# Optimization experiments

Measured on AMD Instinct MI355X. Metric: run time of the kernel, lower is better.

Reference implementation:

```python
import jax, jax.numpy as jnp
import numpy as np
import math

B, T, D = 4, 8192, 1024
EPS = 1e-5

def setup_inputs() -> dict:
    key = jax.random.key(0)
    ks = jax.random.split(key, 8)
    xavier = lambda k, shape: jax.random.uniform(k, shape, jnp.float32,
                                                 -math.sqrt(6.0 / (shape[0] + shape[1])),
                                                 math.sqrt(6.0 / (shape[0] + shape[1])))
    x = jax.random.normal(ks[0], (B, T, D), jnp.float32)
    ln_gamma = jnp.ones((D,), jnp.float32)
    ln_beta = jnp.zeros((D,), jnp.float32)
    Wg = xavier(ks[1], (D, D))            # torch Linear weight: (out, in)
    bg = jnp.zeros((D,), jnp.float32)
    Wv = 0.01 * xavier(ks[2], (D, D))     # gain=0.01
    bv = jnp.zeros((D,), jnp.float32)
    Wo = 0.01 * xavier(ks[3], (D, D))     # gain=0.01
    bo = jnp.zeros((D,), jnp.float32)
    log_decay = jnp.asarray(math.log(math.exp(0.01) - 1.0), jnp.float32)
    return {"x": x, "ln_gamma": ln_gamma, "ln_beta": ln_beta,
            "Wg": Wg, "bg": bg, "Wv": Wv, "bv": bv, "Wo": Wo, "bo": bo,
            "log_decay": log_decay}

def reference(x, ln_gamma, ln_beta, Wg, bg, Wv, bv, Wo, bo, log_decay):
    # LayerNorm
    mu = jnp.mean(x, axis=-1, keepdims=True)
    var = jnp.mean(jnp.square(x - mu), axis=-1, keepdims=True)
    normed = (x - mu) * jax.lax.rsqrt(var + EPS) * ln_gamma + ln_beta
    # gate / value projections (torch Linear: y = x @ W.T + b)
    g = jax.nn.sigmoid(jnp.einsum('btd,ed->bte', normed, Wg) + bg)
    v = jnp.einsum('btd,ed->bte', normed, Wv) + bv
    # push-pull cumulative sums over time
    cumsum = jnp.cumsum(g * v, axis=1) - jnp.cumsum((1.0 - g) * v, axis=1)
    # positional exponential decay
    alpha = jax.nn.softplus(log_decay)
    positions = jnp.arange(x.shape[1], dtype=jnp.float32)
    decay = jnp.exp(-alpha * positions)[None, :, None]  # (1,T,1)
    out = jnp.einsum('btd,ed->bte', cumsum * decay, Wo) + bo
    return x + out  # dropout is identity at eval
```

## Files before the change

kernel.cpp:

```cpp
#include <hip/hip_runtime.h>
#include <cstdint>
#include <cstddef>

#define DD 1024
#define TT 8192
#define BB 4
#define MM (BB*TT)
#define NCHUNK 64
#define CLEN 128
#define EPS 1e-5f
#define NKT 32

typedef __attribute__((ext_vector_type(8))) short bf16x8;
typedef __attribute__((ext_vector_type(4))) float f32x4;

__device__ __forceinline__ float bf2f(unsigned short b) {
  union { unsigned int u; float f; } c; c.u = ((unsigned int)b) << 16; return c.f;
}
__device__ __forceinline__ unsigned short f2bf(float f) {
  union { float f; unsigned int u; } c; c.f = f;
  unsigned int lsb = (c.u >> 16) & 1u;
  c.u += 0x7fffu + lsb;
  return (unsigned short)(c.u >> 16);
}

__device__ __forceinline__ void gload16(const void* gsrc, void* ldst) {
  __builtin_amdgcn_global_load_lds(
      (const __attribute__((address_space(1))) unsigned int*)gsrc,
      (__attribute__((address_space(3))) unsigned int*)ldst, 16, 0, 0);
}

#define SWZ(row) (((row) >> 1) & 3)

__device__ __forceinline__ bf16x8 ldsfrag(const unsigned short* lds, int row, int sl) {
  int sp = sl ^ SWZ(row);
  return *(const bf16x8*)&lds[row * 32 + sp * 8];
}

#define MFMA16(a, b, c) __builtin_amdgcn_mfma_f32_16x16x32_bf16((a), (b), (c), 0, 0, 0)

#define VMCNT0 asm volatile("s_waitcnt vmcnt(0)" ::: "memory")
#define BAR    __builtin_amdgcn_s_barrier()

__global__ __launch_bounds__(256) void cast_weights(
    const float* __restrict__ wg, const float* __restrict__ wv,
    const float* __restrict__ wo,
    unsigned short* __restrict__ owg, unsigned short* __restrict__ owv,
    unsigned short* __restrict__ owo) {
  int i = blockIdx.x * 256 + threadIdx.x;
  const float* src; unsigned short* dst; int off;
  if (i < 262144)       { src = wg; dst = owg; off = i; }
  else if (i < 524288)  { src = wv; dst = owv; off = i - 262144; }
  else                  { src = wo; dst = owo; off = i - 524288; }
  float4 v = ((const float4*)src)[off];
  ushort4 o;
  o.x = f2bf(v.x); o.y = f2bf(v.y); o.z = f2bf(v.z); o.w = f2bf(v.w);
  ((ushort4*)dst)[off] = o;
}

__global__ __launch_bounds__(256) void ln_kernel(
    const float* __restrict__ x, const float* __restrict__ gamma,
    const float* __restrict__ beta, unsigned short* __restrict__ normed) {
  size_t row = blockIdx.x;
  int tid = threadIdx.x, lane = tid & 63, wid = tid >> 6;
  float4 v = ((const float4*)(x + row * DD))[tid];
  float s = v.x + v.y + v.z + v.w;
  float q = v.x * v.x + v.y * v.y + v.z * v.z + v.w * v.w;
#pragma unroll
  for (int off = 32; off; off >>= 1) {
    s += __shfl_down(s, off);
    q += __shfl_down(q, off);
  }
  __shared__ float rs[4], rq[4];
  if (lane == 0) { rs[wid] = s; rq[wid] = q; }
  __syncthreads();
  float ts = rs[0] + rs[1] + rs[2] + rs[3];
  float tq = rq[0] + rq[1] + rq[2] + rq[3];
  float mu  = ts * (1.0f / DD);
  float var = tq * (1.0f / DD) - mu * mu;
  float rstd = rsqrtf(var + EPS);
  float4 gm = ((const float4*)gamma)[tid];
  float4 bt = ((const float4*)beta)[tid];
  ushort4 o;
  o.x = f2bf((v.x - mu) * rstd * gm.x + bt.x);
  o.y = f2bf((v.y - mu) * rstd * gm.y + bt.y);
  o.z = f2bf((v.z - mu) * rstd * gm.z + bt.z);
  o.w = f2bf((v.w - mu) * rstd * gm.w + bt.w);
  ((ushort4*)normed)[row * (DD / 4) + tid] = o;
}

__global__ __launch_bounds__(1024, 4) void gemm_gv(
    const unsigned short* __restrict__ normed,
    const unsigned short* __restrict__ wg, const unsigned short* __restrict__ wv,
    const float* __restrict__ bg, const float* __restrict__ bv,
    unsigned short* __restrict__ u, float* __restrict__ sums) {
  __shared__ unsigned short As[2][256 * 32];
  __shared__ unsigned short Bgs[2][128 * 32];
  __shared__ unsigned short Bvs[2][128 * 32];
  int tid = threadIdx.x, lane = tid & 63, wid = tid >> 6;
  int wm = wid >> 2, wn = wid & 3;
  int nwg = gridDim.x;
  int swz = (blockIdx.x & 7) * (nwg >> 3) + (blockIdx.x >> 3);
  int bx = swz >> 3;
  int by = swz & 7;
  size_t m0 = (size_t)bx * 256;
  int n0 = by * 128;

  int rowA = tid >> 2, spA = tid & 3;
  int slA = spA ^ SWZ(rowA);
  const unsigned short* eA = normed + (m0 + rowA) * DD + slA * 8;
  int lowhalf = (tid < 512);
  int rtid = lowhalf ? tid : tid - 512;
  int rowB = rtid >> 2, spB = rtid & 3;
  int slB = spB ^ SWZ(rowB);
  const unsigned short* eB =
      (lowhalf ? wg : wv) + ((size_t)n0 + rowB) * DD + slB * 8;

  f32x4 accg[4][2], accv[4][2];
#pragma unroll
  for (int a = 0; a < 4; ++a)
#pragma unroll
    for (int b = 0; b < 2; ++b) {
      accg[a][b] = (f32x4){0.f, 0.f, 0.f, 0.f};
      accv[a][b] = (f32x4){0.f, 0.f, 0.f, 0.f};
    }

  gload16(eA, (char*)&As[0][0] + tid * 16);
  gload16(eB, (lowhalf ? (char*)&Bgs[0][0] : (char*)&Bvs[0][0]) + rtid * 16);
  VMCNT0;
  BAR;

  int r = lane & 15, q = lane >> 4;
  for (int t = 0; t < NKT; ++t) {
    int buf = t & 1;
    bool more = (t + 1 < NKT);
    if (more) {
      gload16(eA + (t + 1) * 32, (char*)&As[buf ^ 1][0] + tid * 16);
      gload16(eB + (t + 1) * 32,
              (lowhalf ? (char*)&Bgs[buf ^ 1][0] : (char*)&Bvs[buf ^ 1][0]) + rtid * 16);
    }
    bf16x8 af[4];
#pragma unroll
    for (int mi = 0; mi < 4; ++mi)
      af[mi] = ldsfrag(As[buf], wm * 64 + mi * 16 + r, q);
    bf16x8 g0 = ldsfrag(Bgs[buf], wn * 32 + r, q);
    bf16x8 g1 = ldsfrag(Bgs[buf], wn * 32 + 16 + r, q);
    bf16x8 v0 = ldsfrag(Bvs[buf], wn * 32 + r, q);
    bf16x8 v1 = ldsfrag(Bvs[buf], wn * 32 + 16 + r, q);
    __builtin_amdgcn_s_setprio(1);
#pragma unroll
    for (int mi = 0; mi < 4; ++mi) {
      accg[mi][0] = MFMA16(af[mi], g0, accg[mi][0]);
      accg[mi][1] = MFMA16(af[mi], g1, accg[mi][1]);
      accv[mi][0] = MFMA16(af[mi], v0, accv[mi][0]);
      accv[mi][1] = MFMA16(af[mi], v1, accv[mi][1]);
    }
    __builtin_amdgcn_s_setprio(0);
    if (more) { VMCNT0; BAR; }
  }

  float psum[2] = {0.f, 0.f};
#pragma unroll
  for (int mi = 0; mi < 4; ++mi)
#pragma unroll
    for (int ni = 0; ni < 2; ++ni) {
      int e = n0 + wn * 32 + ni * 16 + r;
      size_t rbase = m0 + wm * 64 + mi * 16 + q * 4;
      float bgv = bg[e], bvv = bv[e];
#pragma unroll
      for (int j = 0; j < 4; ++j) {
        float gp = accg[mi][ni][j] + bgv;
        float vp = accv[mi][ni][j] + bvv;
        float sg = 1.0f / (1.0f + __expf(-gp));
        float uu = (2.0f * sg - 1.0f) * vp;
        psum[ni] += uu;
        u[(rbase + j) * DD + e] = f2bf(uu);
      }
    }
#pragma unroll
  for (int ni = 0; ni < 2; ++ni) {
    psum[ni] += __shfl_xor(psum[ni], 16);
    psum[ni] += __shfl_xor(psum[ni], 32);
  }
  float* S = (float*)&As[0][0];
  BAR;
  if (lane < 16) {
    S[wm * 128 + wn * 32 + lane]      = psum[0];
    S[wm * 128 + wn * 32 + 16 + lane] = psum[1];
  }
  BAR;
  if (tid < 256) {
    int chh = tid >> 7, col = tid & 127;
    float vsum = S[(chh * 2) * 128 + col] + S[(chh * 2 + 1) * 128 + col];
    int b = (int)(m0 >> 13);
    int ch = (int)((m0 & 8191) >> 7) + chh;
    sums[((size_t)(b * NCHUNK + ch)) * DD + n0 + col] = vsum;
  }
}

__global__ __launch_bounds__(256) void scan_chunks(float* __restrict__ sums) {
  int b = blockIdx.x >> 2;
  int e = (blockIdx.x & 3) * 256 + threadIdx.x;
  float vals[NCHUNK];
#pragma unroll
  for (int c = 0; c < NCHUNK; ++c)
    vals[c] = sums[((size_t)(b * NCHUNK + c)) * DD + e];
  float carry = 0.f;
#pragma unroll
  for (int c = 0; c < NCHUNK; ++c) {
    float t = vals[c]; vals[c] = carry; carry += t;
  }
#pragma unroll
  for (int c = 0; c < NCHUNK; ++c)
    sums[((size_t)(b * NCHUNK + c)) * DD + e] = vals[c];
}

__global__ __launch_bounds__(128) void scan_final(
    unsigned short* __restrict__ u, const float* __restrict__ sums,
    const float* __restrict__ log_decay) {
  int bid = blockIdx.x;
  int half = bid & 1, chunk = (bid >> 1) & 63, b = bid >> 7;
  int e0 = half * 512 + threadIdx.x * 4;
  float alpha = log1pf(__expf(log_decay[0]));
  float dec  = __expf(-alpha * (float)(chunk * CLEN));
  float step = __expf(-alpha);
  float4 c = *(const float4*)(sums + ((size_t)(b * NCHUNK + chunk)) * DD + e0);
  size_t base = ((size_t)b * TT + (size_t)chunk * CLEN) * DD + e0;
#pragma unroll 4
  for (int i = 0; i < CLEN; ++i) {
    ushort4 w = *(const ushort4*)(u + base + (size_t)i * DD);
    c.x += bf2f(w.x); c.y += bf2f(w.y); c.z += bf2f(w.z); c.w += bf2f(w.w);
    ushort4 o;
    o.x = f2bf(c.x * dec); o.y = f2bf(c.y * dec);
    o.z = f2bf(c.z * dec); o.w = f2bf(c.w * dec);
    *(ushort4*)(u + base + (size_t)i * DD) = o;
    dec *= step;
  }
}

__global__ __launch_bounds__(1024, 4) void gemm_out(
    const unsigned short* __restrict__ cmat, const unsigned short* __restrict__ wo,
    const float* __restrict__ bo, const float* __restrict__ x,
    float* __restrict__ out) {
  __shared__ unsigned short As[2][256 * 32];
  __shared__ unsigned short Bs[2][256 * 32];
  int tid = threadIdx.x, lane = tid & 63, wid = tid >> 6;
  int wm = wid >> 2, wn = wid & 3;
  int nwg = gridDim.x;
  int swz = (blockIdx.x & 7) * (nwg >> 3) + (blockIdx.x >> 3);
  int bx = swz >> 2;
  int by = swz & 3;
  size_t m0 = (size_t)bx * 256;
  int n0 = by * 256;

  int rowA = tid >> 2, spA = tid & 3;
  int slA = spA ^ SWZ(rowA);
  const unsigned short* eA = cmat + (m0 + rowA) * DD + slA * 8;
  const unsigned short* eB = wo + ((size_t)n0 + rowA) * DD + slA * 8;

  f32x4 acc[4][4];
#pragma unroll
  for (int a = 0; a < 4; ++a)
#pragma unroll
    for (int b = 0; b < 4; ++b) acc[a][b] = (f32x4){0.f, 0.f, 0.f, 0.f};

  gload16(eA, (char*)&As[0][0] + tid * 16);
  gload16(eB, (char*)&Bs[0][0] + tid * 16);
  VMCNT0;
  BAR;

  int r = lane & 15, q = lane >> 4;
  for (int t = 0; t < NKT; ++t) {
    int buf = t & 1;
    bool more = (t + 1 < NKT);
    if (more) {
      gload16(eA + (t + 1) * 32, (char*)&As[buf ^ 1][0] + tid * 16);
      gload16(eB + (t + 1) * 32, (char*)&Bs[buf ^ 1][0] + tid * 16);
    }
    bf16x8 af[4];
#pragma unroll
    for (int mi = 0; mi < 4; ++mi)
      af[mi] = ldsfrag(As[buf], wm * 64 + mi * 16 + r, q);
    bf16x8 b0 = ldsfrag(Bs[buf], wn * 64 + r, q);
    bf16x8 b1 = ldsfrag(Bs[buf], wn * 64 + 16 + r, q);
    bf16x8 b2 = ldsfrag(Bs[buf], wn * 64 + 32 + r, q);
    bf16x8 b3 = ldsfrag(Bs[buf], wn * 64 + 48 + r, q);
    __builtin_amdgcn_s_setprio(1);
#pragma unroll
    for (int mi = 0; mi < 4; ++mi) {
      acc[mi][0] = MFMA16(af[mi], b0, acc[mi][0]);
      acc[mi][1] = MFMA16(af[mi], b1, acc[mi][1]);
      acc[mi][2] = MFMA16(af[mi], b2, acc[mi][2]);
      acc[mi][3] = MFMA16(af[mi], b3, acc[mi][3]);
    }
    __builtin_amdgcn_s_setprio(0);
    if (more) { VMCNT0; BAR; }
  }

#pragma unroll
  for (int mi = 0; mi < 4; ++mi)
#pragma unroll
    for (int nq = 0; nq < 4; ++nq) {
      int e = n0 + wn * 64 + nq * 16 + r;
      size_t rbase = m0 + wm * 64 + mi * 16 + q * 4;
      float bov = bo[e];
#pragma unroll
      for (int j = 0; j < 4; ++j) {
        size_t idx = (rbase + j) * DD + e;
        out[idx] = x[idx] + bov + acc[mi][nq][j];
      }
    }
}

extern "C" void kernel_launch(void* const* d_in, const int* in_sizes, int n_in,
                              void* d_out, int out_size, void* d_ws, size_t ws_size,
                              hipStream_t stream) {
  const float* x     = (const float*)d_in[0];
  const float* gamma = (const float*)d_in[1];
  const float* beta  = (const float*)d_in[2];
  const float* Wg    = (const float*)d_in[3];
  const float* bg    = (const float*)d_in[4];
  const float* Wv    = (const float*)d_in[5];
  const float* bv    = (const float*)d_in[6];
  const float* Wo    = (const float*)d_in[7];
  const float* bo    = (const float*)d_in[8];
  const float* ldcy  = (const float*)d_in[9];
  float* out = (float*)d_out;

  char* ws = (char*)d_ws;
  unsigned short* normed = (unsigned short*)ws;
  unsigned short* u      = (unsigned short*)(ws + (size_t)67108864);
  unsigned short* wgb    = (unsigned short*)(ws + (size_t)134217728);
  unsigned short* wvb    = wgb + 1048576;
  unsigned short* wob    = wvb + 1048576;
  float* sums            = (float*)(ws + (size_t)134217728 + (size_t)3 * 2097152);

  cast_weights<<<3072, 256, 0, stream>>>(Wg, Wv, Wo, wgb, wvb, wob);
  ln_kernel<<<MM, 256, 0, stream>>>(x, gamma, beta, normed);
  gemm_gv<<<dim3(MM / 256 * (DD / 128)), 1024, 0, stream>>>(normed, wgb, wvb, bg, bv, u, sums);
  scan_chunks<<<BB * (DD / 256), 256, 0, stream>>>(sums);
  scan_final<<<BB * NCHUNK * 2, 128, 0, stream>>>(u, sums, ldcy);
  gemm_out<<<dim3(MM / 256 * (DD / 256)), 1024, 0, stream>>>(u, wob, bo, x, out);
}
```

Before: 355.3 us.

## Restructure both GEMMs into 8-wave ping-pong schedule with K=64 tiles

Both GEMM kernels drop from 16 waves to 8 waves per block. Each wave now owns a 128-row slice and computes it in quadrant sub-tiles. K tiles grow to 64 with an XOR row swizzle, and global-to-LDS loads are interleaved between barrier-separated MFMA phases using partial vmcnt waits and setprio. The aim is to overlap memory with matrix math and cut per-iteration barrier overhead, at the cost of more registers per wave, more barriers per outer iteration, and lower occupancy.

```diff
diff --git a/kernel.cpp b/kernel.cpp
--- a/kernel.cpp
+++ b/kernel.cpp
@@ -9,7 +9,7 @@
 #define NCHUNK 64
 #define CLEN 128
 #define EPS 1e-5f
-#define NKT 32
+#define NIT 8
 
 typedef __attribute__((ext_vector_type(8))) short bf16x8;
 typedef __attribute__((ext_vector_type(4))) float f32x4;
@@ -30,17 +30,15 @@
       (__attribute__((address_space(3))) unsigned int*)ldst, 16, 0, 0);
 }
 
-#define SWZ(row) (((row) >> 1) & 3)
-
-__device__ __forceinline__ bf16x8 ldsfrag(const unsigned short* lds, int row, int sl) {
-  int sp = sl ^ SWZ(row);
-  return *(const bf16x8*)&lds[row * 32 + sp * 8];
-}
-
 #define MFMA16(a, b, c) __builtin_amdgcn_mfma_f32_16x16x32_bf16((a), (b), (c), 0, 0, 0)
-
-#define VMCNT0 asm volatile("s_waitcnt vmcnt(0)" ::: "memory")
 #define BAR    __builtin_amdgcn_s_barrier()
+#define PRIO1  __builtin_amdgcn_s_setprio(1)
+#define PRIO0  __builtin_amdgcn_s_setprio(0)
+#define VMW(N) asm volatile("s_waitcnt vmcnt(" #N ")" ::: "memory")
+
+__device__ __forceinline__ bf16x8 FR(const unsigned short* base, int row, int s8) {
+  return *(const bf16x8*)&base[row * 64 + ((s8 ^ (row & 7)) << 3)];
+}
 
 __global__ __launch_bounds__(256) void cast_weights(
     const float* __restrict__ wg, const float* __restrict__ wv,
@@ -89,83 +87,191 @@
   ((ushort4*)normed)[row * (DD / 4) + tid] = o;
 }
 
-__global__ __launch_bounds__(1024, 4) void gemm_gv(
+__global__ __launch_bounds__(512, 2) void gemm_gv(
     const unsigned short* __restrict__ normed,
     const unsigned short* __restrict__ wg, const unsigned short* __restrict__ wv,
     const float* __restrict__ bg, const float* __restrict__ bv,
     unsigned short* __restrict__ u, float* __restrict__ sums) {
-  __shared__ unsigned short As[2][256 * 32];
-  __shared__ unsigned short Bgs[2][128 * 32];
-  __shared__ unsigned short Bvs[2][128 * 32];
+  __shared__ unsigned short As[2][2][128 * 64];
+  __shared__ unsigned short Bgs[2][128 * 64];
+  __shared__ unsigned short Bvs[2][128 * 64];
   int tid = threadIdx.x, lane = tid & 63, wid = tid >> 6;
   int wm = wid >> 2, wn = wid & 3;
-  int nwg = gridDim.x;
-  int swz = (blockIdx.x & 7) * (nwg >> 3) + (blockIdx.x >> 3);
-  int bx = swz >> 3;
-  int by = swz & 7;
+  int swz = (blockIdx.x & 7) * (gridDim.x >> 3) + (blockIdx.x >> 3);
+  int bx = swz >> 3, by = swz & 7;
   size_t m0 = (size_t)bx * 256;
   int n0 = by * 128;
 
-  int rowA = tid >> 2, spA = tid & 3;
-  int slA = spA ^ SWZ(rowA);
-  const unsigned short* eA = normed + (m0 + rowA) * DD + slA * 8;
-  int lowhalf = (tid < 512);
-  int rtid = lowhalf ? tid : tid - 512;
-  int rowB = rtid >> 2, spB = rtid & 3;
-  int slB = spB ^ SWZ(rowB);
-  const unsigned short* eB =
-      (lowhalf ? wg : wv) + ((size_t)n0 + rowB) * DD + slB * 8;
-
-  f32x4 accg[4][2], accv[4][2];
-#pragma unroll
-  for (int a = 0; a < 4; ++a)
+  int ua = tid, ub = tid + 512;
+  int ra = ua >> 3, sa = (ua & 7) ^ (ra & 7);
+  int rb = ub >> 3, sb = (ub & 7) ^ (rb & 7);
+  const unsigned short* gA = normed + m0 * DD;
+  const unsigned short* gBg = wg + (size_t)n0 * DD;
+  const unsigned short* gBv = wv + (size_t)n0 * DD;
+  auto SA = [&](int t, int h) {
+    const unsigned short* s = gA + (size_t)h * 128 * DD + t * 64;
+    char* d = (char*)&As[t & 1][h][0];
+    gload16(s + (size_t)ra * DD + sa * 8, d + ua * 16);
+    gload16(s + (size_t)rb * DD + sb * 8, d + ub * 16);
+  };
+  auto SG = [&](int t) {
+    char* d = (char*)&Bgs[t & 1][0];
+    gload16(gBg + (size_t)ra * DD + t * 64 + sa * 8, d + ua * 16);
+    gload16(gBg + (size_t)rb * DD + t * 64 + sb * 8, d + ub * 16);
+  };
+  auto SV = [&](int t) {
+    char* d = (char*)&Bvs[t & 1][0];
+    gload16(gBv + (size_t)ra * DD + t * 64 + sa * 8, d + ua * 16);
+    gload16(gBv + (size_t)rb * DD + t * 64 + sb * 8, d + ub * 16);
+  };
+
+  f32x4 accg[8][2], accv[8][2];
+#pragma unroll
+  for (int a = 0; a < 8; ++a)
 #pragma unroll
     for (int b = 0; b < 2; ++b) {
       accg[a][b] = (f32x4){0.f, 0.f, 0.f, 0.f};
       accv[a][b] = (f32x4){0.f, 0.f, 0.f, 0.f};
     }
 
-  gload16(eA, (char*)&As[0][0] + tid * 16);
-  gload16(eB, (lowhalf ? (char*)&Bgs[0][0] : (char*)&Bvs[0][0]) + rtid * 16);
-  VMCNT0;
+  SG(0); SV(0); SA(0, 0); SA(0, 1); SG(1); SV(1); SA(1, 0);
+  VMW(6);
   BAR;
 
   int r = lane & 15, q = lane >> 4;
-  for (int t = 0; t < NKT; ++t) {
-    int buf = t & 1;
-    bool more = (t + 1 < NKT);
-    if (more) {
-      gload16(eA + (t + 1) * 32, (char*)&As[buf ^ 1][0] + tid * 16);
-      gload16(eB + (t + 1) * 32,
-              (lowhalf ? (char*)&Bgs[buf ^ 1][0] : (char*)&Bvs[buf ^ 1][0]) + rtid * 16);
-    }
-    bf16x8 af[4];
-#pragma unroll
-    for (int mi = 0; mi < 4; ++mi)
-      af[mi] = ldsfrag(As[buf], wm * 64 + mi * 16 + r, q);
-    bf16x8 g0 = ldsfrag(Bgs[buf], wn * 32 + r, q);
-    bf16x8 g1 = ldsfrag(Bgs[buf], wn * 32 + 16 + r, q);
-    bf16x8 v0 = ldsfrag(Bvs[buf], wn * 32 + r, q);
-    bf16x8 v1 = ldsfrag(Bvs[buf], wn * 32 + 16 + r, q);
-    __builtin_amdgcn_s_setprio(1);
-#pragma unroll
-    for (int mi = 0; mi < 4; ++mi) {
-      accg[mi][0] = MFMA16(af[mi], g0, accg[mi][0]);
-      accg[mi][1] = MFMA16(af[mi], g1, accg[mi][1]);
-      accv[mi][0] = MFMA16(af[mi], v0, accv[mi][0]);
-      accv[mi][1] = MFMA16(af[mi], v1, accv[mi][1]);
-    }
-    __builtin_amdgcn_s_setprio(0);
-    if (more) { VMCNT0; BAR; }
+  bf16x8 am[4][2], bgf[2][2], bvf[2][2];
+  for (int T = 0; T < NIT; ++T) {
+    bool more = (T < NIT - 1);
+    int t1 = 2 * T + 1, t2 = 2 * T + 2, t3 = 2 * T + 3;
+#pragma unroll
+    for (int mi = 0; mi < 4; ++mi)
+#pragma unroll
+      for (int kk = 0; kk < 2; ++kk)
+        am[mi][kk] = FR(As[0][wm], mi * 16 + r, kk * 4 + q);
+#pragma unroll
+    for (int ni = 0; ni < 2; ++ni)
+#pragma unroll
+      for (int kk = 0; kk < 2; ++kk)
+        bgf[ni][kk] = FR(Bgs[0], wn * 32 + ni * 16 + r, kk * 4 + q);
+    SA(t1, 1);
+    BAR; PRIO1;
+#pragma unroll
+    for (int mi = 0; mi < 4; ++mi)
+#pragma unroll
+      for (int ni = 0; ni < 2; ++ni)
+#pragma unroll
+        for (int kk = 0; kk < 2; ++kk)
+          accg[mi][ni] = MFMA16(am[mi][kk], bgf[ni][kk], accg[mi][ni]);
+    PRIO0; BAR;
+#pragma unroll
+    for (int ni = 0; ni < 2; ++ni)
+#pragma unroll
+      for (int kk = 0; kk < 2; ++kk)
+        bvf[ni][kk] = FR(Bvs[0], wn * 32 + ni * 16 + r, kk * 4 + q);
+    if (more) SG(t2);
+    BAR; PRIO1;
+#pragma unroll
+    for (int mi = 0; mi < 4; ++mi)
+#pragma unroll
+      for (int ni = 0; ni < 2; ++ni)
+#pragma unroll
+        for (int kk = 0; kk < 2; ++kk)
+          accv[mi][ni] = MFMA16(am[mi][kk], bvf[ni][kk], accv[mi][ni]);
+    PRIO0; BAR;
+#pragma unroll
+    for (int mi = 0; mi < 4; ++mi)
+#pragma unroll
+      for (int kk = 0; kk < 2; ++kk)
+        am[mi][kk] = FR(As[0][wm], 64 + mi * 16 + r, kk * 4 + q);
+    if (more) SV(t2);
+    BAR; PRIO1;
+#pragma unroll
+    for (int mi = 0; mi < 4; ++mi)
+#pragma unroll
+      for (int ni = 0; ni < 2; ++ni)
+#pragma unroll
+        for (int kk = 0; kk < 2; ++kk)
+          accv[4 + mi][ni] = MFMA16(am[mi][kk], bvf[ni][kk], accv[4 + mi][ni]);
+    PRIO0; BAR;
+    if (more) { SA(t2, 0); VMW(6); } else { VMW(0); }
+    BAR; PRIO1;
+#pragma unroll
+    for (int mi = 0; mi < 4; ++mi)
+#pragma unroll
+      for (int ni = 0; ni < 2; ++ni)
+#pragma unroll
+        for (int kk = 0; kk < 2; ++kk)
+          accg[4 + mi][ni] = MFMA16(am[mi][kk], bgf[ni][kk], accg[4 + mi][ni]);
+    PRIO0; BAR;
+#pragma unroll
+    for (int mi = 0; mi < 4; ++mi)
+#pragma unroll
+      for (int kk = 0; kk < 2; ++kk)
+        am[mi][kk] = FR(As[1][wm], mi * 16 + r, kk * 4 + q);
+#pragma unroll
+    for (int ni = 0; ni < 2; ++ni)
+#pragma unroll
+      for (int kk = 0; kk < 2; ++kk)
+        bgf[ni][kk] = FR(Bgs[1], wn * 32 + ni * 16 + r, kk * 4 + q);
+    if (more) SA(t2, 1);
+    BAR; PRIO1;
+#pragma unroll
+    for (int mi = 0; mi < 4; ++mi)
+#pragma unroll
+      for (int ni = 0; ni < 2; ++ni)
+#pragma unroll
+        for (int kk = 0; kk < 2; ++kk)
+          accg[mi][ni] = MFMA16(am[mi][kk], bgf[ni][kk], accg[mi][ni]);
+    PRIO0; BAR;
+#pragma unroll
+    for (int ni = 0; ni < 2; ++ni)
+#pragma unroll
+      for (int kk = 0; kk < 2; ++kk)
+        bvf[ni][kk] = FR(Bvs[1], wn * 32 + ni * 16 + r, kk * 4 + q);
+    if (more) SG(t3);
+    BAR; PRIO1;
+#pragma unroll
+    for (int mi = 0; mi < 4; ++mi)
+#pragma unroll
+      for (int ni = 0; ni < 2; ++ni)
+#pragma unroll
+        for (int kk = 0; kk < 2; ++kk)
+          accv[mi][ni] = MFMA16(am[mi][kk], bvf[ni][kk], accv[mi][ni]);
+    PRIO0; BAR;
+#pragma unroll
+    for (int mi = 0; mi < 4; ++mi)
+#pragma unroll
+      for (int kk = 0; kk < 2; ++kk)
+        am[mi][kk] = FR(As[1][wm], 64 + mi * 16 + r, kk * 4 + q);
+    if (more) SV(t3);
+    BAR; PRIO1;
+#pragma unroll
+    for (int mi = 0; mi < 4; ++mi)
+#pragma unroll
+      for (int ni = 0; ni < 2; ++ni)
+#pragma unroll
+        for (int kk = 0; kk < 2; ++kk)
+          accv[4 + mi][ni] = MFMA16(am[mi][kk], bvf[ni][kk], accv[4 + mi][ni]);
+    PRIO0; BAR;
+    if (more) { SA(t3, 0); VMW(6); } else { VMW(0); }
+    BAR; PRIO1;
+#pragma unroll
+    for (int mi = 0; mi < 4; ++mi)
+#pragma unroll
+      for (int ni = 0; ni < 2; ++ni)
+#pragma unroll
+        for (int kk = 0; kk < 2; ++kk)
+          accg[4 + mi][ni] = MFMA16(am[mi][kk], bgf[ni][kk], accg[4 + mi][ni]);
+    PRIO0; BAR;
   }
 
   float psum[2] = {0.f, 0.f};
 #pragma unroll
-  for (int mi = 0; mi < 4; ++mi)
+  for (int mi = 0; mi < 8; ++mi)
 #pragma unroll
     for (int ni = 0; ni < 2; ++ni) {
       int e = n0 + wn * 32 + ni * 16 + r;
-      size_t rbase = m0 + wm * 64 + mi * 16 + q * 4;
+      size_t rbase = m0 + wm * 128 + mi * 16 + q * 4;
       float bgv = bg[e], bvv = bv[e];
 #pragma unroll
       for (int j = 0; j < 4; ++j) {
@@ -182,19 +288,12 @@
     psum[ni] += __shfl_xor(psum[ni], 16);
     psum[ni] += __shfl_xor(psum[ni], 32);
   }
-  float* S = (float*)&As[0][0];
-  BAR;
   if (lane < 16) {
-    S[wm * 128 + wn * 32 + lane]      = psum[0];
-    S[wm * 128 + wn * 32 + 16 + lane] = psum[1];
-  }
-  BAR;
-  if (tid < 256) {
-    int chh = tid >> 7, col = tid & 127;
-    float vsum = S[(chh * 2) * 128 + col] + S[(chh * 2 + 1) * 128 + col];
     int b = (int)(m0 >> 13);
-    int ch = (int)((m0 & 8191) >> 7) + chh;
-    sums[((size_t)(b * NCHUNK + ch)) * DD + n0 + col] = vsum;
+    int ch = (int)((m0 & 8191) >> 7) + wm;
+    size_t sidx = ((size_t)(b * NCHUNK + ch)) * DD + n0 + wn * 32 + lane;
+    sums[sidx]      = psum[0];
+    sums[sidx + 16] = psum[1];
   }
 }
 
@@ -238,71 +337,181 @@
   }
 }
 
-__global__ __launch_bounds__(1024, 4) void gemm_out(
+__global__ __launch_bounds__(512, 2) void gemm_out(
     const unsigned short* __restrict__ cmat, const unsigned short* __restrict__ wo,
     const float* __restrict__ bo, const float* __restrict__ x,
     float* __restrict__ out) {
-  __shared__ unsigned short As[2][256 * 32];
-  __shared__ unsigned short Bs[2][256 * 32];
+  __shared__ unsigned short As[2][2][128 * 64];
+  __shared__ unsigned short Bs[2][2][128 * 64];
   int tid = threadIdx.x, lane = tid & 63, wid = tid >> 6;
   int wm = wid >> 2, wn = wid & 3;
-  int nwg = gridDim.x;
-  int swz = (blockIdx.x & 7) * (nwg >> 3) + (blockIdx.x >> 3);
-  int bx = swz >> 2;
-  int by = swz & 3;
+  int swz = (blockIdx.x & 7) * (gridDim.x >> 3) + (blockIdx.x >> 3);
+  int bx = swz >> 2, by = swz & 3;
   size_t m0 = (size_t)bx * 256;
   int n0 = by * 256;
-
-  int rowA = tid >> 2, spA = tid & 3;
-  int slA = spA ^ SWZ(rowA);
-  const unsigned short* eA = cmat + (m0 + rowA) * DD + slA * 8;
-  const unsigned short* eB = wo + ((size_t)n0 + rowA) * DD + slA * 8;
-
-  f32x4 acc[4][4];
-#pragma unroll
-  for (int a = 0; a < 4; ++a)
+  int bh = wn >> 1, nb = wn & 1;
+
+  int ua = tid, ub = tid + 512;
+  int ra = ua >> 3, sa = (ua & 7) ^ (ra & 7);
+  int rb = ub >> 3, sb = (ub & 7) ^ (rb & 7);
+  const unsigned short* gA = cmat + m0 * DD;
+  const unsigned short* gB = wo + (size_t)n0 * DD;
+  auto SA = [&](int t, int h) {
+    const unsigned short* s = gA + (size_t)h * 128 * DD + t * 64;
+    char* d = (char*)&As[t & 1][h][0];
+    gload16(s + (size_t)ra * DD + sa * 8, d + ua * 16);
+    gload16(s + (size_t)rb * DD + sb * 8, d + ub * 16);
+  };
+  auto SB = [&](int t, int h) {
+    const unsigned short* s = gB + (size_t)h * 128 * DD + t * 64;
+    char* d = (char*)&Bs[t & 1][h][0];
+    gload16(s + (size_t)ra * DD + sa * 8, d + ua * 16);
+    gload16(s + (size_t)rb * DD + sb * 8, d + ub * 16);
+  };
+
+  f32x4 acc[8][4];
+#pragma unroll
+  for (int a = 0; a < 8; ++a)
 #pragma unroll
     for (int b = 0; b < 4; ++b) acc[a][b] = (f32x4){0.f, 0.f, 0.f, 0.f};
 
-  gload16(eA, (char*)&As[0][0] + tid * 16);
-  gload16(eB, (char*)&Bs[0][0] + tid * 16);
-  VMCNT0;
+  SB(0, 0); SB(0, 1); SA(0, 0); SA(0, 1); SB(1, 0); SB(1, 1);
+  VMW(4);
   BAR;
 
   int r = lane & 15, q = lane >> 4;
-  for (int t = 0; t < NKT; ++t) {
-    int buf = t & 1;
-    bool more = (t + 1 < NKT);
-    if (more) {
-      gload16(eA + (t + 1) * 32, (char*)&As[buf ^ 1][0] + tid * 16);
-      gload16(eB + (t + 1) * 32, (char*)&Bs[buf ^ 1][0] + tid * 16);
-    }
-    bf16x8 af[4];
-#pragma unroll
-    for (int mi = 0; mi < 4; ++mi)
-      af[mi] = ldsfrag(As[buf], wm * 64 + mi * 16 + r, q);
-    bf16x8 b0 = ldsfrag(Bs[buf], wn * 64 + r, q);
-    bf16x8 b1 = ldsfrag(Bs[buf], wn * 64 + 16 + r, q);
-    bf16x8 b2 = ldsfrag(Bs[buf], wn * 64 + 32 + r, q);
-    bf16x8 b3 = ldsfrag(Bs[buf], wn * 64 + 48 + r, q);
-    __builtin_amdgcn_s_setprio(1);
-#pragma unroll
-    for (int mi = 0; mi < 4; ++mi) {
-      acc[mi][0] = MFMA16(af[mi], b0, acc[mi][0]);
-      acc[mi][1] = MFMA16(af[mi], b1, acc[mi][1]);
-      acc[mi][2] = MFMA16(af[mi], b2, acc[mi][2]);
-      acc[mi][3] = MFMA16(af[mi], b3, acc[mi][3]);
-    }
-    __builtin_amdgcn_s_setprio(0);
-    if (more) { VMCNT0; BAR; }
-  }
-
-#pragma unroll
-  for (int mi = 0; mi < 4; ++mi)
+  bf16x8 am[4][2], b01[2][2], b23[2][2];
+  for (int T = 0; T < NIT; ++T) {
+    bool more = (T < NIT - 1);
+    int t1 = 2 * T + 1, t2 = 2 * T + 2, t3 = 2 * T + 3;
+#pragma unroll
+    for (int mi = 0; mi < 4; ++mi)
+#pragma unroll
+      for (int kk = 0; kk < 2; ++kk)
+        am[mi][kk] = FR(As[0][wm], mi * 16 + r, kk * 4 + q);
+#pragma unroll
+    for (int ni = 0; ni < 2; ++ni)
+#pragma unroll
+      for (int kk = 0; kk < 2; ++kk)
+        b01[ni][kk] = FR(Bs[0][bh], nb * 64 + ni * 16 + r, kk * 4 + q);
+    SA(t1, 0);
+    BAR; PRIO1;
+#pragma unroll
+    for (int mi = 0; mi < 4; ++mi)
+#pragma unroll
+      for (int ni = 0; ni < 2; ++ni)
+#pragma unroll
+        for (int kk = 0; kk < 2; ++kk)
+          acc[mi][ni] = MFMA16(am[mi][kk], b01[ni][kk], acc[mi][ni]);
+    PRIO0; BAR;
+#pragma unroll
+    for (int ni = 0; ni < 2; ++ni)
+#pragma unroll
+      for (int kk = 0; kk < 2; ++kk)
+        b23[ni][kk] = FR(Bs[0][bh], nb * 64 + 32 + ni * 16 + r, kk * 4 + q);
+    SA(t1, 1);
+    BAR; PRIO1;
+#pragma unroll
+    for (int mi = 0; mi < 4; ++mi)
+#pragma unroll
+      for (int ni = 0; ni < 2; ++ni)
+#pragma unroll
+        for (int kk = 0; kk < 2; ++kk)
+          acc[mi][2 + ni] = MFMA16(am[mi][kk], b23[ni][kk], acc[mi][2 + ni]);
+    PRIO0; BAR;
+#pragma unroll
+    for (int mi = 0; mi < 4; ++mi)
+#pragma unroll
+      for (int kk = 0; kk < 2; ++kk)
+        am[mi][kk] = FR(As[0][wm], 64 + mi * 16 + r, kk * 4 + q);
+    if (more) SB(t2, 0);
+    BAR; PRIO1;
+#pragma unroll
+    for (int mi = 0; mi < 4; ++mi)
+#pragma unroll
+      for (int ni = 0; ni < 2; ++ni)
+#pragma unroll
+        for (int kk = 0; kk < 2; ++kk)
+          acc[4 + mi][2 + ni] = MFMA16(am[mi][kk], b23[ni][kk], acc[4 + mi][2 + ni]);
+    PRIO0; BAR;
+    if (more) { SB(t2, 1); VMW(4); } else { VMW(0); }
+    BAR; PRIO1;
+#pragma unroll
+    for (int mi = 0; mi < 4; ++mi)
+#pragma unroll
+      for (int ni = 0; ni < 2; ++ni)
+#pragma unroll
+        for (int kk = 0; kk < 2; ++kk)
+          acc[4 + mi][ni] = MFMA16(am[mi][kk], b01[ni][kk], acc[4 + mi][ni]);
+    PRIO0; BAR;
+#pragma unroll
+    for (int mi = 0; mi < 4; ++mi)
+#pragma unroll
+      for (int kk = 0; kk < 2; ++kk)
+        am[mi][kk] = FR(As[1][wm], mi * 16 + r, kk * 4 + q);
+#pragma unroll
+    for (int ni = 0; ni < 2; ++ni)
+#pragma unroll
+      for (int kk = 0; kk < 2; ++kk)
+        b01[ni][kk] = FR(Bs[1][bh], nb * 64 + ni * 16 + r, kk * 4 + q);
+    if (more) SA(t2, 0);
+    BAR; PRIO1;
+#pragma unroll
+    for (int mi = 0; mi < 4; ++mi)
+#pragma unroll
+      for (int ni = 0; ni < 2; ++ni)
+#pragma unroll
+        for (int kk = 0; kk < 2; ++kk)
+          acc[mi][ni] = MFMA16(am[mi][kk], b01[ni][kk], acc[mi][ni]);
+    PRIO0; BAR;
+#pragma unroll
+    for (int ni = 0; ni < 2; ++ni)
+#pragma unroll
+      for (int kk = 0; kk < 2; ++kk)
+        b23[ni][kk] = FR(Bs[1][bh], nb * 64 + 32 + ni * 16 + r, kk * 4 + q);
+    if (more) SA(t2, 1);
+    BAR; PRIO1;
+#pragma unroll
+    for (int mi = 0; mi < 4; ++mi)
+#pragma unroll
+      for (int ni = 0; ni < 2; ++ni)
+#pragma unroll
+        for (int kk = 0; kk < 2; ++kk)
+          acc[mi][2 + ni] = MFMA16(am[mi][kk], b23[ni][kk], acc[mi][2 + ni]);
+    PRIO0; BAR;
+#pragma unroll
+    for (int mi = 0; mi < 4; ++mi)
+#pragma unroll
+      for (int kk = 0; kk < 2; ++kk)
+        am[mi][kk] = FR(As[1][wm], 64 + mi * 16 + r, kk * 4 + q);
+    if (more) SB(t3, 0);
+    BAR; PRIO1;
+#pragma unroll
+    for (int mi = 0; mi < 4; ++mi)
+#pragma unroll
+      for (int ni = 0; ni < 2; ++ni)
+#pragma unroll
+        for (int kk = 0; kk < 2; ++kk)
+          acc[4 + mi][2 + ni] = MFMA16(am[mi][kk], b23[ni][kk], acc[4 + mi][2 + ni]);
+    PRIO0; BAR;
+    if (more) { SB(t3, 1); VMW(4); } else { VMW(0); }
+    BAR; PRIO1;
+#pragma unroll
+    for (int mi = 0; mi < 4; ++mi)
+#pragma unroll
+      for (int ni = 0; ni < 2; ++ni)
+#pragma unroll
+        for (int kk = 0; kk < 2; ++kk)
+          acc[4 + mi][ni] = MFMA16(am[mi][kk], b01[ni][kk], acc[4 + mi][ni]);
+    PRIO0; BAR;
+  }
+
+#pragma unroll
+  for (int mi = 0; mi < 8; ++mi)
 #pragma unroll
     for (int nq = 0; nq < 4; ++nq) {
       int e = n0 + wn * 64 + nq * 16 + r;
-      size_t rbase = m0 + wm * 64 + mi * 16 + q * 4;
+      size_t rbase = m0 + wm * 128 + mi * 16 + q * 4;
       float bov = bo[e];
 #pragma unroll
       for (int j = 0; j < 4; ++j) {
@@ -337,8 +546,8 @@
 
   cast_weights<<<3072, 256, 0, stream>>>(Wg, Wv, Wo, wgb, wvb, wob);
   ln_kernel<<<MM, 256, 0, stream>>>(x, gamma, beta, normed);
-  gemm_gv<<<dim3(MM / 256 * (DD / 128)), 1024, 0, stream>>>(normed, wgb, wvb, bg, bv, u, sums);
+  gemm_gv<<<dim3(MM / 256 * (DD / 128)), 512, 0, stream>>>(normed, wgb, wvb, bg, bv, u, sums);
   scan_chunks<<<BB * (DD / 256), 256, 0, stream>>>(sums);
   scan_final<<<BB * NCHUNK * 2, 128, 0, stream>>>(u, sums, ldcy);
-  gemm_out<<<dim3(MM / 256 * (DD / 256)), 1024, 0, stream>>>(u, wob, bo, x, out);
-}
+  gemm_out<<<dim3(MM / 256 * (DD / 256)), 512, 0, stream>>>(u, wob, bo, x, out);
+}
```

Measured after the change: 335.5 us. 5.6% less time.
